# Kernel tuning notes

Measured on AMD Instinct MI355X. Metric: run time of the kernel, lower is better.

The kernel has to match this reference:

```python
import jax, jax.numpy as jnp
import numpy as np

EPS = 1e-5

def conv1x1(x, W, b):
    # x: [B,Cin,H,W], W: [Cout,Cin], b: [Cout] -> [B,Cout,H,W]
    return jnp.einsum('oc,bchw->bohw', W, x) + b[None, :, None, None]

def setup_inputs() -> dict:
    key = jax.random.key(0)
    ks = jax.random.split(key, 12)
    C, Ci = 256, 128
    B, Hh, Wh, Hl, Wl = 8, 32, 32, 64, 64
    sc = 1.0 / np.sqrt(C)
    sci = 1.0 / np.sqrt(Ci)
    return {
        'x_high': jax.random.normal(ks[0], (B, C, Hh, Wh), jnp.float32),
        'x_low':  jax.random.normal(ks[1], (B, C, Hl, Wl), jnp.float32),
        'Wg': jax.random.normal(ks[2], (Ci, C), jnp.float32) * sc,
        'bg': jax.random.normal(ks[3], (Ci,), jnp.float32) * 0.01,
        'Wt': jax.random.normal(ks[4], (Ci, C), jnp.float32) * sc,
        'bt': jax.random.normal(ks[5], (Ci,), jnp.float32) * 0.01,
        'Wp': jax.random.normal(ks[6], (Ci, C), jnp.float32) * sc,
        'bp': jax.random.normal(ks[7], (Ci,), jnp.float32) * 0.01,
        'Wz': jax.random.normal(ks[8], (C, Ci), jnp.float32) * sci,
        'bz': jax.random.normal(ks[9], (C,), jnp.float32) * 0.01,
        'gamma': jnp.ones((C,), jnp.float32),
        'beta': jnp.zeros((C,), jnp.float32),
    }

def reference(x_high, x_low, Wg, bg, Wt, bt, Wp, bp, Wz, bz, gamma, beta):
    B, C, Hl, Wl = x_low.shape
    Ci = Wg.shape[0]
    Nh = x_high.shape[2] * x_high.shape[3]
    Nl = Hl * Wl
    # 1x1 conv projections (pure channel GEMMs)
    g_x = conv1x1(x_high, Wg, bg).reshape(B, Ci, Nh).transpose(0, 2, 1)    # [B,Nh,Ci]
    theta_x = conv1x1(x_low, Wt, bt).reshape(B, Ci, Nl).transpose(0, 2, 1) # [B,Nl,Ci]
    phi_x = conv1x1(x_high, Wp, bp).reshape(B, Ci, Nh)                     # [B,Ci,Nh]
    # unnormalized attention (no softmax), scaled by number of key positions
    f = jnp.matmul(theta_x, phi_x)            # [B,Nl,Nh]
    y = jnp.matmul(f / Nh, g_x)               # [B,Nl,Ci]
    y = y.transpose(0, 2, 1).reshape(B, Ci, Hl, Wl)
    # W_z: 1x1 conv then GroupNorm(num_groups=1) -> layernorm over (C,H,W) per sample
    z = conv1x1(y, Wz, bz)                    # [B,C,Hl,Wl]
    mu = jnp.mean(z, axis=(1, 2, 3), keepdims=True)
    var = jnp.var(z, axis=(1, 2, 3), keepdims=True)
    z = (z - mu) * jax.lax.rsqrt(var + EPS)
    z = z * gamma[None, :, None, None] + beta[None, :, None, None]
    return z
```

## Files before the change

### kernel.cpp

```cpp
#include <hip/hip_runtime.h>
#include <hip/hip_bf16.h>

typedef __attribute__((ext_vector_type(8))) short bf16x8;
typedef __attribute__((ext_vector_type(4))) float f32x4;
typedef __attribute__((ext_vector_type(4))) unsigned short us4;
typedef __attribute__((ext_vector_type(8))) unsigned short us8;

#define MFMA(a, b, c) __builtin_amdgcn_mfma_f32_16x16x32_bf16(a, b, c, 0, 0, 0)

__device__ inline unsigned short f2bf(float f) {
  unsigned u = __builtin_bit_cast(unsigned, f);
  u += 0x7FFF + ((u >> 16) & 1);
  return (unsigned short)(u >> 16);
}
__device__ inline float bf2f(unsigned short s) {
  unsigned u = ((unsigned)s) << 16;
  return __builtin_bit_cast(float, u);
}
__device__ inline unsigned pack2(float lo, float hi) {
  return (unsigned)f2bf(lo) | ((unsigned)f2bf(hi) << 16);
}
__device__ inline void gll16(const unsigned short* gsrc, unsigned short* ldst) {
  __builtin_amdgcn_global_load_lds(
      (const __attribute__((address_space(1))) unsigned int*)gsrc,
      (__attribute__((address_space(3))) unsigned int*)ldst, 16, 0, 0);
}

__global__ __launch_bounds__(256) void cvt_w2(
    const float* __restrict__ A, const float* __restrict__ B,
    unsigned short* __restrict__ Ab, unsigned short* __restrict__ Bb) {
  int i = blockIdx.x * 256 + threadIdx.x;
  float4 a = *(const float4*)&A[i * 4];
  float4 b = *(const float4*)&B[i * 4];
  us4 ua, ub;
  ua[0] = f2bf(a.x); ua[1] = f2bf(a.y); ua[2] = f2bf(a.z); ua[3] = f2bf(a.w);
  ub[0] = f2bf(b.x); ub[1] = f2bf(b.y); ub[2] = f2bf(b.z); ub[3] = f2bf(b.w);
  *(us4*)&Ab[i * 4] = ua;
  *(us4*)&Bb[i * 4] = ub;
}

__global__ __launch_bounds__(256) void proj_f(
    const float* __restrict__ xh,
    const unsigned short* __restrict__ Wpb, const float* __restrict__ bp,
    const unsigned short* __restrict__ Wgb, const float* __restrict__ bg,
    unsigned short* __restrict__ phi,
    unsigned short* __restrict__ gg) {
  __shared__ unsigned short Bs[64 * 256];
  __shared__ unsigned short As[2][128 * 64];
  const int b = blockIdx.x, n0 = blockIdx.y * 64;
  const int t = threadIdx.x, lane = t & 63;
  const int wid = t >> 6, wr = wid >> 1, wc = wid & 1;
  #pragma unroll
  for (int it = 0; it < 8; ++it) {
    int s = it * 256 + t;
    int nf = (s & 7) | ((s >> 10) << 3);
    int c2 = (s >> 3) & 127;
    const float* p = xh + ((size_t)(b * 256 + 2 * c2)) * 1024 + n0 + nf * 4;
    float4 a = *(const float4*)p;
    float4 bq = *(const float4*)(p + 1024);
    const float* ap = (const float*)&a;
    const float* bp2 = (const float*)&bq;
    #pragma unroll
    for (int i = 0; i < 4; ++i) {
      int n = nf * 4 + i;
      int col32 = (((c2 >> 2) ^ (n & 7)) << 2) | (c2 & 3);
      ((unsigned*)Bs)[n * 128 + col32] = pack2(ap[i], bp2[i]);
    }
  }
  f32x4 accP[4][2] = {};
  f32x4 accG[4][2] = {};
  for (int kt = 0; kt < 4; ++kt) {
    #pragma unroll
    for (int p = 0; p < 2; ++p) {
      const unsigned short* W = p ? Wgb : Wpb;
      #pragma unroll
      for (int j = 0; j < 4; ++j) {
        int slot = t + j * 256;
        int r = slot >> 3, gq = slot & 7;
        gll16(W + (size_t)r * 256 + kt * 64 + (gq ^ (r & 7)) * 8,
              As[p] + slot * 8);
      }
    }
    __syncthreads();
    #pragma unroll
    for (int ks = 0; ks < 2; ++ks) {
      bf16x8 bfr[2];
      #pragma unroll
      for (int fm = 0; fm < 2; ++fm) {
        int r = wc * 32 + fm * 16 + (lane & 15);
        int gc = kt * 8 + ks * 4 + (lane >> 4);
        bfr[fm] = *(const bf16x8*)&Bs[r * 256 + (gc ^ (r & 7)) * 8];
      }
      #pragma unroll
      for (int fo = 0; fo < 4; ++fo) {
        int r = wr * 64 + fo * 16 + (lane & 15);
        int ga = ks * 4 + (lane >> 4);
        bf16x8 ap = *(const bf16x8*)&As[0][r * 64 + (ga ^ (r & 7)) * 8];
        bf16x8 ag = *(const bf16x8*)&As[1][r * 64 + (ga ^ (r & 7)) * 8];
        accP[fo][0] = MFMA(ap, bfr[0], accP[fo][0]);
        accP[fo][1] = MFMA(ap, bfr[1], accP[fo][1]);
        accG[fo][0] = MFMA(ag, bfr[0], accG[fo][0]);
        accG[fo][1] = MFMA(ag, bfr[1], accG[fo][1]);
      }
    }
    __syncthreads();
  }
  #pragma unroll
  for (int fo = 0; fo < 4; ++fo) {
    #pragma unroll
    for (int q = 0; q < 4; ++q) {
      int i = wr * 64 + fo * 16 + (lane >> 4) * 4 + q;
      float vp = bp[i], vg = bg[i];
      #pragma unroll
      for (int fm = 0; fm < 2; ++fm) {
        int n = n0 + wc * 32 + fm * 16 + (lane & 15);
        size_t off = ((size_t)(b * 128 + i)) * 1024 + n;
        phi[off] = f2bf(accP[fo][fm][q] + vp);
        gg[off]  = f2bf(accG[fo][fm][q] + vg);
      }
    }
  }
}

__global__ __launch_bounds__(256) void mpart_mfma(
    const unsigned short* __restrict__ phi, const unsigned short* __restrict__ gg,
    float* __restrict__ Mpart) {
  __shared__ unsigned short ps[128 * 128];
  __shared__ unsigned short gs[128 * 128];
  const int b = blockIdx.x, kc = blockIdx.y;
  const int t = threadIdx.x, lane = t & 63;
  const int wid = t >> 6, wr = wid >> 1, wc = wid & 1;
  #pragma unroll
  for (int j = 0; j < 8; ++j) {
    int slot = t + j * 256;
    int r = slot >> 4, gq = slot & 15;
    size_t src = ((size_t)(b * 128 + r)) * 1024 + kc * 128 + (gq ^ (r & 7)) * 8;
    gll16(phi + src, ps + slot * 8);
    gll16(gg + src, gs + slot * 8);
  }
  __syncthreads();
  f32x4 acc[4][4] = {};
  #pragma unroll
  for (int ks = 0; ks < 4; ++ks) {
    bf16x8 av[4], bv[4];
    #pragma unroll
    for (int f = 0; f < 4; ++f) {
      int ra = wr * 64 + f * 16 + (lane & 15);
      int rb = wc * 64 + f * 16 + (lane & 15);
      int gc = ks * 4 + (lane >> 4);
      av[f] = *(const bf16x8*)&ps[ra * 128 + (gc ^ (ra & 7)) * 8];
      bv[f] = *(const bf16x8*)&gs[rb * 128 + (gc ^ (rb & 7)) * 8];
    }
    #pragma unroll
    for (int i = 0; i < 4; ++i)
      #pragma unroll
      for (int j2 = 0; j2 < 4; ++j2)
        acc[i][j2] = MFMA(av[i], bv[j2], acc[i][j2]);
  }
  float* mp = Mpart + ((size_t)(b * 8 + kc)) * 128 * 128;
  #pragma unroll
  for (int i = 0; i < 4; ++i)
    #pragma unroll
    for (int q = 0; q < 4; ++q) {
      int ii = wr * 64 + i * 16 + (lane >> 4) * 4 + q;
      #pragma unroll
      for (int j2 = 0; j2 < 4; ++j2) {
        int jj = wc * 64 + j2 * 16 + (lane & 15);
        mp[ii * 128 + jj] = acc[i][j2][q];
      }
    }
}

__global__ __launch_bounds__(256) void mreduce(
    const float* __restrict__ Mpart, float* __restrict__ M) {
  int i4 = blockIdx.x * 256 + threadIdx.x;
  int b = i4 >> 12, r4 = i4 & 4095;
  const float4* p = (const float4*)Mpart + (size_t)b * 8 * 4096 + r4;
  float4 s = {0.f, 0.f, 0.f, 0.f};
  #pragma unroll
  for (int kc = 0; kc < 8; ++kc) {
    float4 v = p[(size_t)kc * 4096];
    s.x += v.x; s.y += v.y; s.z += v.z; s.w += v.w;
  }
  const float sc = 1.0f / 1024.0f;
  s.x *= sc; s.y *= sc; s.z *= sc; s.w *= sc;
  ((float4*)M)[i4] = s;
}

__global__ __launch_bounds__(256) void mk_K(
    const float* __restrict__ M, const float* __restrict__ Wz,
    float* __restrict__ K) {
  const int b = blockIdx.x, o0 = blockIdx.y * 32;
  const int t = threadIdx.x;
  const int i = t & 127, og = (t >> 7) * 16;
  float acc[16] = {};
  const float* mrow = M + ((size_t)(b * 128 + i)) * 128;
  for (int j = 0; j < 128; j += 4) {
    float4 m4 = *(const float4*)&mrow[j];
    #pragma unroll
    for (int o = 0; o < 16; ++o) {
      float4 w4 = *(const float4*)&Wz[(o0 + og + o) * 128 + j];
      acc[o] += m4.x * w4.x + m4.y * w4.y + m4.z * w4.z + m4.w * w4.w;
    }
  }
  #pragma unroll
  for (int o = 0; o < 16; ++o)
    K[((size_t)(b * 256 + o0 + og + o)) * 128 + i] = acc[o];
}

__global__ __launch_bounds__(256) void mk_W2(
    const float* __restrict__ K, const float* __restrict__ Wt,
    const float* __restrict__ bt, const float* __restrict__ bz,
    unsigned short* __restrict__ W2b, float* __restrict__ b2) {
  __shared__ float Ks[32 * 128];
  const int b = blockIdx.x, o0 = blockIdx.y * 32;
  const int t = threadIdx.x;
  #pragma unroll
  for (int k = 0; k < 4; ++k) {
    int f = t + k * 256;
    int o = f >> 5, q = (f & 31) << 2;
    *(float4*)&Ks[o * 128 + q] = *(const float4*)&K[((size_t)(b * 256 + o0 + o)) * 128 + q];
  }
  __syncthreads();
  const int c = t;
  float acc[32] = {};
  for (int i = 0; i < 128; i += 4) {
    float w0 = Wt[(i + 0) * 256 + c];
    float w1 = Wt[(i + 1) * 256 + c];
    float w2 = Wt[(i + 2) * 256 + c];
    float w3 = Wt[(i + 3) * 256 + c];
    #pragma unroll
    for (int o = 0; o < 32; ++o) {
      float4 k4 = *(const float4*)&Ks[o * 128 + i];
      acc[o] += k4.x * w0 + k4.y * w1 + k4.z * w2 + k4.w * w3;
    }
  }
  #pragma unroll
  for (int o = 0; o < 32; ++o)
    W2b[((size_t)(b * 256 + o0 + o)) * 256 + c] = f2bf(acc[o]);
  if (t < 32) {
    float s = 0.f;
    for (int i = 0; i < 128; ++i) s += Ks[t * 128 + i] * bt[i];
    b2[b * 256 + o0 + t] = s + bz[o0 + t];
  }
}

__global__ __launch_bounds__(256) void mk_z_f(
    const float* __restrict__ xl,
    const unsigned short* __restrict__ W2b,
    const float* __restrict__ b2,
    unsigned short* __restrict__ z,
    float* __restrict__ sums) {
  __shared__ unsigned short As[256 * 64];
  __shared__ unsigned short Bs[64 * 64];
  __shared__ float red[8];
  const int b = blockIdx.x, m0 = blockIdx.y * 64;
  const int t = threadIdx.x, lane = t & 63;
  const int w = t >> 6;
  f32x4 acc[4][4] = {};
  for (int kt = 0; kt < 4; ++kt) {
    #pragma unroll
    for (int j = 0; j < 8; ++j) {
      int slot = t + j * 256;
      int r = slot >> 3, gq = slot & 7;
      gll16(W2b + ((size_t)(b * 256 + r)) * 256 + kt * 64 + (gq ^ (r & 7)) * 8,
            As + slot * 8);
    }
    #pragma unroll
    for (int it = 0; it < 2; ++it) {
      int s = it * 256 + t;
      int mf = (s & 7) | ((s >> 8) << 3);
      int c2 = (s >> 3) & 31;
      const float* p = xl + ((size_t)(b * 256 + kt * 64 + 2 * c2)) * 4096 + m0 + mf * 4;
      float4 a = *(const float4*)p;
      float4 bq = *(const float4*)(p + 4096);
      const float* ap = (const float*)&a;
      const float* bp2 = (const float*)&bq;
      #pragma unroll
      for (int i = 0; i < 4; ++i) {
        int m = mf * 4 + i;
        int col32 = (((c2 >> 2) ^ (m & 7)) << 2) | (c2 & 3);
        ((unsigned*)Bs)[m * 32 + col32] = pack2(ap[i], bp2[i]);
      }
    }
    __syncthreads();
    #pragma unroll
    for (int ks = 0; ks < 2; ++ks) {
      bf16x8 av[4], bv[4];
      #pragma unroll
      for (int f = 0; f < 4; ++f) {
        int ra = w * 64 + f * 16 + (lane & 15);
        int rb = f * 16 + (lane & 15);
        int gc = ks * 4 + (lane >> 4);
        av[f] = *(const bf16x8*)&As[ra * 64 + (gc ^ (ra & 7)) * 8];
        bv[f] = *(const bf16x8*)&Bs[rb * 64 + (gc ^ (rb & 7)) * 8];
      }
      #pragma unroll
      for (int i = 0; i < 4; ++i)
        #pragma unroll
        for (int j2 = 0; j2 < 4; ++j2)
          acc[i][j2] = MFMA(av[i], bv[j2], acc[i][j2]);
    }
    __syncthreads();
  }
  float ls = 0.f, ls2 = 0.f;
  #pragma unroll
  for (int i = 0; i < 4; ++i) {
    #pragma unroll
    for (int q = 0; q < 4; ++q) {
      int o = w * 64 + i * 16 + (lane >> 4) * 4 + q;
      float bias = b2[b * 256 + o];
      #pragma unroll
      for (int j2 = 0; j2 < 4; ++j2) {
        int m = m0 + j2 * 16 + (lane & 15);
        float v = acc[i][j2][q] + bias;
        z[((size_t)(b * 256 + o)) * 4096 + m] = f2bf(v);
        ls += v; ls2 += v * v;
      }
    }
  }
  #pragma unroll
  for (int off = 32; off > 0; off >>= 1) {
    ls  += __shfl_down(ls, off);
    ls2 += __shfl_down(ls2, off);
  }
  if ((t & 63) == 0) { red[w * 2] = ls; red[w * 2 + 1] = ls2; }
  __syncthreads();
  if (t == 0) {
    atomicAdd(&sums[b * 2 + 0], red[0] + red[2] + red[4] + red[6]);
    atomicAdd(&sums[b * 2 + 1], red[1] + red[3] + red[5] + red[7]);
  }
}

__global__ __launch_bounds__(256) void ln_out(
    const unsigned short* __restrict__ z, const float* __restrict__ sums,
    const float* __restrict__ gamma, const float* __restrict__ beta,
    float* __restrict__ out) {
  size_t i8 = (size_t)blockIdx.x * 256 + threadIdx.x;
  int b = (int)(i8 >> 17);
  int o = (int)((i8 >> 9) & 255);
  float s = sums[b * 2], s2 = sums[b * 2 + 1];
  const float invN = 1.0f / (256.0f * 4096.0f);
  float mu = s * invN;
  float var = s2 * invN - mu * mu;
  float rs = rsqrtf(var + 1e-5f);
  float ga = gamma[o] * rs;
  float be = beta[o] - mu * rs * gamma[o];
  us8 u = *(const us8*)&z[i8 * 8];
  float4 r0, r1;
  r0.x = bf2f(u[0]) * ga + be; r0.y = bf2f(u[1]) * ga + be;
  r0.z = bf2f(u[2]) * ga + be; r0.w = bf2f(u[3]) * ga + be;
  r1.x = bf2f(u[4]) * ga + be; r1.y = bf2f(u[5]) * ga + be;
  r1.z = bf2f(u[6]) * ga + be; r1.w = bf2f(u[7]) * ga + be;
  *(float4*)&out[i8 * 8] = r0;
  *(float4*)&out[i8 * 8 + 4] = r1;
}

extern "C" void kernel_launch(void* const* d_in, const int* in_sizes, int n_in,
                              void* d_out, int out_size, void* d_ws, size_t ws_size,
                              hipStream_t stream) {
  const float* xh    = (const float*)d_in[0];
  const float* xl    = (const float*)d_in[1];
  const float* Wg    = (const float*)d_in[2];
  const float* bg    = (const float*)d_in[3];
  const float* Wt    = (const float*)d_in[4];
  const float* bt    = (const float*)d_in[5];
  const float* Wp    = (const float*)d_in[6];
  const float* bp    = (const float*)d_in[7];
  const float* Wz    = (const float*)d_in[8];
  const float* bz    = (const float*)d_in[9];
  const float* gamma = (const float*)d_in[10];
  const float* beta  = (const float*)d_in[11];
  float* out = (float*)d_out;
  float* ws = (float*)d_ws;

  unsigned short* phi  = (unsigned short*)(ws + 0);
  unsigned short* gbuf = (unsigned short*)(ws + 524288);
  float* Mpart = ws + 1048576;
  float* M     = ws + 2097152;
  float* K     = ws + 2228224;
  unsigned short* zbuf = (unsigned short*)(ws + 0);
  unsigned short* W2b  = (unsigned short*)(ws + 4194304);
  float* b2    = ws + 4456448;
  float* sums  = ws + 4458496;
  unsigned short* Wpb  = (unsigned short*)(ws + 4458512);
  unsigned short* Wgb  = (unsigned short*)(ws + 4474896);

  hipMemsetAsync(sums, 0, 16 * sizeof(float), stream);

  cvt_w2<<<32, 256, 0, stream>>>(Wp, Wg, Wpb, Wgb);
  proj_f<<<dim3(8, 16), 256, 0, stream>>>(xh, Wpb, bp, Wgb, bg, phi, gbuf);
  mpart_mfma<<<dim3(8, 8), 256, 0, stream>>>(phi, gbuf, Mpart);
  mreduce<<<128, 256, 0, stream>>>(Mpart, M);
  mk_K<<<dim3(8, 8), 256, 0, stream>>>(M, Wz, K);
  mk_W2<<<dim3(8, 8), 256, 0, stream>>>(K, Wt, bt, bz, W2b, b2);
  mk_z_f<<<dim3(8, 64), 256, 0, stream>>>(xl, W2b, b2, zbuf, sums);
  ln_out<<<4096, 256, 0, stream>>>(zbuf, sums, gamma, beta, out);
}
```

Baseline: 207.3 us.

## Fuse weight conversion, M reduction and K/W2 building; split projection and z tiles

The projection kernel now reads fp32 Wp/Wg directly and converts them while staging to LDS, which removes the separate conversion launch. It is also split over output-channel halves to double the grid. The Mpart reduction, the K=Wz·M product and the W2 construction are merged into one kernel that keeps M and K in padded shared memory, removing two launches and their global round trips. The z GEMM tile is halved along the spatial axis to double the block count. The trade-off is redundant work: each projection block converts its own weights and reloads its x_high tile, and each mkw2 block re-reduces the full M per batch.

```diff
diff --git a/kernel.cpp b/kernel.cpp
--- a/kernel.cpp
+++ b/kernel.cpp
@@ -3,7 +3,6 @@
 
 typedef __attribute__((ext_vector_type(8))) short bf16x8;
 typedef __attribute__((ext_vector_type(4))) float f32x4;
-typedef __attribute__((ext_vector_type(4))) unsigned short us4;
 typedef __attribute__((ext_vector_type(8))) unsigned short us8;
 
 #define MFMA(a, b, c) __builtin_amdgcn_mfma_f32_16x16x32_bf16(a, b, c, 0, 0, 0)
@@ -26,28 +25,15 @@
       (__attribute__((address_space(3))) unsigned int*)ldst, 16, 0, 0);
 }
 
-__global__ __launch_bounds__(256) void cvt_w2(
-    const float* __restrict__ A, const float* __restrict__ B,
-    unsigned short* __restrict__ Ab, unsigned short* __restrict__ Bb) {
-  int i = blockIdx.x * 256 + threadIdx.x;
-  float4 a = *(const float4*)&A[i * 4];
-  float4 b = *(const float4*)&B[i * 4];
-  us4 ua, ub;
-  ua[0] = f2bf(a.x); ua[1] = f2bf(a.y); ua[2] = f2bf(a.z); ua[3] = f2bf(a.w);
-  ub[0] = f2bf(b.x); ub[1] = f2bf(b.y); ub[2] = f2bf(b.z); ub[3] = f2bf(b.w);
-  *(us4*)&Ab[i * 4] = ua;
-  *(us4*)&Bb[i * 4] = ub;
-}
-
-__global__ __launch_bounds__(256) void proj_f(
+__global__ __launch_bounds__(256) void proj_f2(
     const float* __restrict__ xh,
-    const unsigned short* __restrict__ Wpb, const float* __restrict__ bp,
-    const unsigned short* __restrict__ Wgb, const float* __restrict__ bg,
+    const float* __restrict__ Wp, const float* __restrict__ bp,
+    const float* __restrict__ Wg, const float* __restrict__ bg,
     unsigned short* __restrict__ phi,
     unsigned short* __restrict__ gg) {
   __shared__ unsigned short Bs[64 * 256];
-  __shared__ unsigned short As[2][128 * 64];
-  const int b = blockIdx.x, n0 = blockIdx.y * 64;
+  __shared__ unsigned short As[2][64 * 64];
+  const int b = blockIdx.x, i0 = blockIdx.y * 64, n0 = blockIdx.z * 64;
   const int t = threadIdx.x, lane = t & 63;
   const int wid = t >> 6, wr = wid >> 1, wc = wid & 1;
   #pragma unroll
@@ -67,18 +53,22 @@
       ((unsigned*)Bs)[n * 128 + col32] = pack2(ap[i], bp2[i]);
     }
   }
-  f32x4 accP[4][2] = {};
-  f32x4 accG[4][2] = {};
+  f32x4 accP[2][2] = {};
+  f32x4 accG[2][2] = {};
+  const int ar = t >> 2, acb = (t & 3) * 16;
   for (int kt = 0; kt < 4; ++kt) {
     #pragma unroll
-    for (int p = 0; p < 2; ++p) {
-      const unsigned short* W = p ? Wgb : Wpb;
-      #pragma unroll
-      for (int j = 0; j < 4; ++j) {
-        int slot = t + j * 256;
-        int r = slot >> 3, gq = slot & 7;
-        gll16(W + (size_t)r * 256 + kt * 64 + (gq ^ (r & 7)) * 8,
-              As[p] + slot * 8);
+    for (int w = 0; w < 2; ++w) {
+      const float* W = (w ? Wg : Wp) + (size_t)(i0 + ar) * 256 + kt * 64 + acb;
+      #pragma unroll
+      for (int q = 0; q < 4; ++q) {
+        float4 v = *(const float4*)(W + q * 4);
+        int cl0 = acb + q * 4;
+        int c2a = cl0 >> 1, c2b = c2a + 1;
+        int sa = (((c2a >> 2) ^ (ar & 7)) << 2) | (c2a & 3);
+        int sb = (((c2b >> 2) ^ (ar & 7)) << 2) | (c2b & 3);
+        ((unsigned*)As[w])[ar * 32 + sa] = pack2(v.x, v.y);
+        ((unsigned*)As[w])[ar * 32 + sb] = pack2(v.z, v.w);
       }
     }
     __syncthreads();
@@ -92,8 +82,8 @@
         bfr[fm] = *(const bf16x8*)&Bs[r * 256 + (gc ^ (r & 7)) * 8];
       }
       #pragma unroll
-      for (int fo = 0; fo < 4; ++fo) {
-        int r = wr * 64 + fo * 16 + (lane & 15);
+      for (int fo = 0; fo < 2; ++fo) {
+        int r = wr * 32 + fo * 16 + (lane & 15);
         int ga = ks * 4 + (lane >> 4);
         bf16x8 ap = *(const bf16x8*)&As[0][r * 64 + (ga ^ (r & 7)) * 8];
         bf16x8 ag = *(const bf16x8*)&As[1][r * 64 + (ga ^ (r & 7)) * 8];
@@ -106,15 +96,15 @@
     __syncthreads();
   }
   #pragma unroll
-  for (int fo = 0; fo < 4; ++fo) {
+  for (int fo = 0; fo < 2; ++fo) {
     #pragma unroll
     for (int q = 0; q < 4; ++q) {
-      int i = wr * 64 + fo * 16 + (lane >> 4) * 4 + q;
+      int i = i0 + wr * 32 + fo * 16 + (lane >> 4) * 4 + q;
       float vp = bp[i], vg = bg[i];
       #pragma unroll
       for (int fm = 0; fm < 2; ++fm) {
         int n = n0 + wc * 32 + fm * 16 + (lane & 15);
-        size_t off = ((size_t)(b * 128 + i)) * 1024 + n;
+        size_t off = ((size_t)((b * 128) + i)) * 1024 + n;
         phi[off] = f2bf(accP[fo][fm][q] + vp);
         gg[off]  = f2bf(accG[fo][fm][q] + vg);
       }
@@ -171,76 +161,66 @@
     }
 }
 
-__global__ __launch_bounds__(256) void mreduce(
-    const float* __restrict__ Mpart, float* __restrict__ M) {
-  int i4 = blockIdx.x * 256 + threadIdx.x;
-  int b = i4 >> 12, r4 = i4 & 4095;
-  const float4* p = (const float4*)Mpart + (size_t)b * 8 * 4096 + r4;
-  float4 s = {0.f, 0.f, 0.f, 0.f};
-  #pragma unroll
-  for (int kc = 0; kc < 8; ++kc) {
-    float4 v = p[(size_t)kc * 4096];
-    s.x += v.x; s.y += v.y; s.z += v.z; s.w += v.w;
-  }
-  const float sc = 1.0f / 1024.0f;
-  s.x *= sc; s.y *= sc; s.z *= sc; s.w *= sc;
-  ((float4*)M)[i4] = s;
-}
-
-__global__ __launch_bounds__(256) void mk_K(
-    const float* __restrict__ M, const float* __restrict__ Wz,
-    float* __restrict__ K) {
+__global__ __launch_bounds__(256) void mkw2(
+    const float* __restrict__ Mpart, const float* __restrict__ Wz,
+    const float* __restrict__ Wt, const float* __restrict__ bt,
+    const float* __restrict__ bz,
+    unsigned short* __restrict__ W2b, float* __restrict__ b2) {
+  __shared__ float Ms[128 * 129];
+  __shared__ float Ws2[32 * 132];
   const int b = blockIdx.x, o0 = blockIdx.y * 32;
   const int t = threadIdx.x;
-  const int i = t & 127, og = (t >> 7) * 16;
-  float acc[16] = {};
-  const float* mrow = M + ((size_t)(b * 128 + i)) * 128;
-  for (int j = 0; j < 128; j += 4) {
-    float4 m4 = *(const float4*)&mrow[j];
-    #pragma unroll
-    for (int o = 0; o < 16; ++o) {
-      float4 w4 = *(const float4*)&Wz[(o0 + og + o) * 128 + j];
-      acc[o] += m4.x * w4.x + m4.y * w4.y + m4.z * w4.z + m4.w * w4.w;
-    }
-  }
-  #pragma unroll
-  for (int o = 0; o < 16; ++o)
-    K[((size_t)(b * 256 + o0 + og + o)) * 128 + i] = acc[o];
-}
-
-__global__ __launch_bounds__(256) void mk_W2(
-    const float* __restrict__ K, const float* __restrict__ Wt,
-    const float* __restrict__ bt, const float* __restrict__ bz,
-    unsigned short* __restrict__ W2b, float* __restrict__ b2) {
-  __shared__ float Ks[32 * 128];
-  const int b = blockIdx.x, o0 = blockIdx.y * 32;
-  const int t = threadIdx.x;
-  #pragma unroll
-  for (int k = 0; k < 4; ++k) {
-    int f = t + k * 256;
-    int o = f >> 5, q = (f & 31) << 2;
-    *(float4*)&Ks[o * 128 + q] = *(const float4*)&K[((size_t)(b * 256 + o0 + o)) * 128 + q];
-  }
+  #pragma unroll
+  for (int q = 0; q < 4; ++q) {
+    int f = t + q * 256;
+    int o = f >> 5, j4 = (f & 31) * 4;
+    float4 v = *(const float4*)&Wz[(size_t)(o0 + o) * 128 + j4];
+    Ws2[o * 132 + j4 + 0] = v.x; Ws2[o * 132 + j4 + 1] = v.y;
+    Ws2[o * 132 + j4 + 2] = v.z; Ws2[o * 132 + j4 + 3] = v.w;
+  }
+  #pragma unroll
+  for (int q = 0; q < 16; ++q) {
+    int f = t + q * 256;
+    const float4* p = (const float4*)(Mpart + (size_t)b * 8 * 16384) + f;
+    float4 s = p[0];
+    #pragma unroll
+    for (int kc = 1; kc < 8; ++kc) {
+      float4 v = p[(size_t)kc * 4096];
+      s.x += v.x; s.y += v.y; s.z += v.z; s.w += v.w;
+    }
+    const float sc = 1.0f / 1024.0f;
+    int i = f >> 5, j = (f & 31) * 4;
+    Ms[i * 129 + j + 0] = s.x * sc; Ms[i * 129 + j + 1] = s.y * sc;
+    Ms[i * 129 + j + 2] = s.z * sc; Ms[i * 129 + j + 3] = s.w * sc;
+  }
+  __syncthreads();
+  const int i = t & 127, oh = t >> 7;
+  float k2[16] = {};
+  for (int j = 0; j < 128; ++j) {
+    float m = Ms[i * 129 + j];
+    #pragma unroll
+    for (int oo = 0; oo < 16; ++oo)
+      k2[oo] += m * Ws2[(oh * 16 + oo) * 132 + j];
+  }
+  __syncthreads();
+  #pragma unroll
+  for (int oo = 0; oo < 16; ++oo)
+    Ws2[(oh * 16 + oo) * 132 + i] = k2[oo];
   __syncthreads();
   const int c = t;
   float acc[32] = {};
-  for (int i = 0; i < 128; i += 4) {
-    float w0 = Wt[(i + 0) * 256 + c];
-    float w1 = Wt[(i + 1) * 256 + c];
-    float w2 = Wt[(i + 2) * 256 + c];
-    float w3 = Wt[(i + 3) * 256 + c];
-    #pragma unroll
-    for (int o = 0; o < 32; ++o) {
-      float4 k4 = *(const float4*)&Ks[o * 128 + i];
-      acc[o] += k4.x * w0 + k4.y * w1 + k4.z * w2 + k4.w * w3;
-    }
+  for (int i2 = 0; i2 < 128; ++i2) {
+    float wt = Wt[(size_t)i2 * 256 + c];
+    #pragma unroll
+    for (int o = 0; o < 32; ++o)
+      acc[o] += wt * Ws2[o * 132 + i2];
   }
   #pragma unroll
   for (int o = 0; o < 32; ++o)
     W2b[((size_t)(b * 256 + o0 + o)) * 256 + c] = f2bf(acc[o]);
   if (t < 32) {
     float s = 0.f;
-    for (int i = 0; i < 128; ++i) s += Ks[t * 128 + i] * bt[i];
+    for (int i2 = 0; i2 < 128; ++i2) s += Ws2[t * 132 + i2] * bt[i2];
     b2[b * 256 + o0 + t] = s + bz[o0 + t];
   }
 }
@@ -252,12 +232,13 @@
     unsigned short* __restrict__ z,
     float* __restrict__ sums) {
   __shared__ unsigned short As[256 * 64];
-  __shared__ unsigned short Bs[64 * 64];
+  __shared__ unsigned short Bs[32 * 64];
   __shared__ float red[8];
-  const int b = blockIdx.x, m0 = blockIdx.y * 64;
+  const int b = blockIdx.x, m0 = blockIdx.y * 32;
   const int t = threadIdx.x, lane = t & 63;
   const int w = t >> 6;
-  f32x4 acc[4][4] = {};
+  const int mf = t & 7, c2 = t >> 3;
+  f32x4 acc[4][2] = {};
   for (int kt = 0; kt < 4; ++kt) {
     #pragma unroll
     for (int j = 0; j < 8; ++j) {
@@ -266,11 +247,7 @@
       gll16(W2b + ((size_t)(b * 256 + r)) * 256 + kt * 64 + (gq ^ (r & 7)) * 8,
             As + slot * 8);
     }
-    #pragma unroll
-    for (int it = 0; it < 2; ++it) {
-      int s = it * 256 + t;
-      int mf = (s & 7) | ((s >> 8) << 3);
-      int c2 = (s >> 3) & 31;
+    {
       const float* p = xl + ((size_t)(b * 256 + kt * 64 + 2 * c2)) * 4096 + m0 + mf * 4;
       float4 a = *(const float4*)p;
       float4 bq = *(const float4*)(p + 4096);
@@ -286,19 +263,23 @@
     __syncthreads();
     #pragma unroll
     for (int ks = 0; ks < 2; ++ks) {
-      bf16x8 av[4], bv[4];
+      bf16x8 av[4], bv[2];
+      #pragma unroll
+      for (int f = 0; f < 2; ++f) {
+        int rb = f * 16 + (lane & 15);
+        int gc = ks * 4 + (lane >> 4);
+        bv[f] = *(const bf16x8*)&Bs[rb * 64 + (gc ^ (rb & 7)) * 8];
+      }
       #pragma unroll
       for (int f = 0; f < 4; ++f) {
         int ra = w * 64 + f * 16 + (lane & 15);
-        int rb = f * 16 + (lane & 15);
         int gc = ks * 4 + (lane >> 4);
         av[f] = *(const bf16x8*)&As[ra * 64 + (gc ^ (ra & 7)) * 8];
-        bv[f] = *(const bf16x8*)&Bs[rb * 64 + (gc ^ (rb & 7)) * 8];
       }
       #pragma unroll
       for (int i = 0; i < 4; ++i)
         #pragma unroll
-        for (int j2 = 0; j2 < 4; ++j2)
+        for (int j2 = 0; j2 < 2; ++j2)
           acc[i][j2] = MFMA(av[i], bv[j2], acc[i][j2]);
     }
     __syncthreads();
@@ -311,7 +292,7 @@
       int o = w * 64 + i * 16 + (lane >> 4) * 4 + q;
       float bias = b2[b * 256 + o];
       #pragma unroll
-      for (int j2 = 0; j2 < 4; ++j2) {
+      for (int j2 = 0; j2 < 2; ++j2) {
         int m = m0 + j2 * 16 + (lane & 15);
         float v = acc[i][j2][q] + bias;
         z[((size_t)(b * 256 + o)) * 4096 + m] = f2bf(v);
@@ -377,23 +358,16 @@
   unsigned short* phi  = (unsigned short*)(ws + 0);
   unsigned short* gbuf = (unsigned short*)(ws + 524288);
   float* Mpart = ws + 1048576;
-  float* M     = ws + 2097152;
-  float* K     = ws + 2228224;
   unsigned short* zbuf = (unsigned short*)(ws + 0);
   unsigned short* W2b  = (unsigned short*)(ws + 4194304);
   float* b2    = ws + 4456448;
   float* sums  = ws + 4458496;
-  unsigned short* Wpb  = (unsigned short*)(ws + 4458512);
-  unsigned short* Wgb  = (unsigned short*)(ws + 4474896);
 
   hipMemsetAsync(sums, 0, 16 * sizeof(float), stream);
 
-  cvt_w2<<<32, 256, 0, stream>>>(Wp, Wg, Wpb, Wgb);
-  proj_f<<<dim3(8, 16), 256, 0, stream>>>(xh, Wpb, bp, Wgb, bg, phi, gbuf);
+  proj_f2<<<dim3(8, 2, 16), 256, 0, stream>>>(xh, Wp, bp, Wg, bg, phi, gbuf);
   mpart_mfma<<<dim3(8, 8), 256, 0, stream>>>(phi, gbuf, Mpart);
-  mreduce<<<128, 256, 0, stream>>>(Mpart, M);
-  mk_K<<<dim3(8, 8), 256, 0, stream>>>(M, Wz, K);
-  mk_W2<<<dim3(8, 8), 256, 0, stream>>>(K, Wt, bt, bz, W2b, b2);
-  mk_z_f<<<dim3(8, 64), 256, 0, stream>>>(xl, W2b, b2, zbuf, sums);
+  mkw2<<<dim3(8, 8), 256, 0, stream>>>(Mpart, Wz, Wt, bt, bz, W2b, b2);
+  mk_z_f<<<dim3(8, 128), 256, 0, stream>>>(xl, W2b, b2, zbuf, sums);
   ln_out<<<4096, 256, 0, stream>>>(zbuf, sums, gamma, beta, out);
 }
```

Result: no change. 209.2 us (+0.9%).
